# Optimization experiments

Measured on AMD Instinct MI355X. Metric: run time of the kernel, lower is better.

The kernel has to match this reference:

```python
import jax, jax.numpy as jnp
import numpy as np

NX = NY = 2048
DT = 0.01
DX = 1.0
DY = 1.0
RE = 1.0
NLEVEL = int(np.log2(NY)) + 1  # 12 levels


def pad_zero(x):
    # Dirichlet (zero) halo of width 1: matches boundary_condition_u/v/k/cw
    return jnp.pad(x, ((0, 0), (0, 0), (1, 1), (1, 1)))


def pad_edge(x):
    # Edge-replicate halo (incl. corners): matches boundary_condition_p
    return jnp.pad(x, ((0, 0), (0, 0), (1, 1), (1, 1)), mode='edge')


def conv2d(x, w, stride=1):
    return jax.lax.conv_general_dilated(
        x, w, (stride, stride), 'VALID',
        dimension_numbers=('NCHW', 'OIHW', 'NCHW'))


def upsample2(x):
    return jnp.repeat(jnp.repeat(x, 2, axis=2), 2, axis=3)


def pg_vector(u, v, pad_u, pad_v, k1, ADx_u, ADy_u, ADx_v, ADy_v, AD2_u, AD2_v, w_diff):
    # Petrov-Galerkin dissipation. pad_u/pad_v are the padded ORIGINAL velocities:
    # the torch code references the global values_uu/values_vv buffers here.
    k_u = 0.25 * DX * jnp.abs(0.5 * DX ** -3 * (jnp.abs(u) * DX + jnp.abs(v) * DY) * AD2_u) \
        / (0.001 + (jnp.abs(ADx_u) * DX ** -3 + jnp.abs(ADy_u) * DX ** -3) / 2.0)
    k_v = 0.25 * DY * jnp.abs(0.5 * DX ** -3 * (jnp.abs(u) * DX + jnp.abs(v) * DY) * AD2_v) \
        / (0.001 + (jnp.abs(ADx_v) * DX ** -3 + jnp.abs(ADy_v) * DX ** -3) / 2.0)
    k_u = jnp.minimum(k_u, k1)
    k_v = jnp.minimum(k_v, k1)
    k_uu = pad_zero(k_u)
    k_vv = pad_zero(k_v)
    k_x = 1.5 * (k_u * AD2_u + conv2d(pad_u * k_uu, w_diff) - u * conv2d(k_uu, w_diff))
    k_y = 1.5 * (k_v * AD2_v + conv2d(pad_v * k_vv, w_diff) - v * conv2d(k_vv, w_diff))
    return k_x, k_y


def f_cycle_mg(pad_u, pad_v, values_p, iteration, w_A, w_res, w_xadv, w_yadv):
    diag = w_A[0, 0, 1, 1]
    b = -(conv2d(pad_u, w_xadv) + conv2d(pad_v, w_yadv)) / DT
    w = jnp.zeros((1, 1, 2, 2), values_p.dtype)
    r = b
    for _ in range(iteration):
        w = jnp.zeros((1, 1, 2, 2), values_p.dtype)
        r = conv2d(pad_edge(values_p), w_A) - b
        r_s = [r]
        for _i in range(1, NLEVEL - 1):
            r = conv2d(r, w_res, stride=2)  # restriction down to 2x2
            r_s.append(r)
        for i in reversed(range(1, NLEVEL - 1)):
            w = w - conv2d(pad_zero(w), w_A) / diag + r_s[i] / diag  # Jacobi smooth
            w = upsample2(w)  # prolongation
        values_p = values_p - w
        values_p = values_p - conv2d(pad_edge(values_p), w_A) / diag + b / diag
    return values_p, w, r


def setup_inputs() -> dict:
    key = jax.random.key(0)
    ku, kv, kp = jax.random.split(key, 3)
    shp = (1, 1, NY, NX)
    f32 = jnp.float32
    values_u = jax.random.normal(ku, shp, f32) * 0.1
    values_v = jax.random.normal(kv, shp, f32) * 0.1
    values_p = jax.random.normal(kp, shp, f32) * 0.1
    Fx = jnp.zeros(shp, f32)
    Fy = jnp.zeros(shp, f32)
    k1 = jnp.ones(shp, f32) * (DX ** 2 / DT)
    # FD stencils (learned conv params in the torch module)
    w_xadv = jnp.array([[0., 0., 0.], [-0.5, 0., 0.5], [0., 0., 0.]], f32).reshape(1, 1, 3, 3) / DX
    w_yadv = jnp.array([[0., -0.5, 0.], [0., 0., 0.], [0., 0.5, 0.]], f32).reshape(1, 1, 3, 3) / DY
    lap = jnp.array([[0., 1., 0.], [1., -4., 1.], [0., 1., 0.]], f32).reshape(1, 1, 3, 3) / DX ** 2
    w_diff = lap
    w_A = lap  # diag = -4
    w_res = jnp.full((1, 1, 2, 2), 0.25, f32)
    return dict(values_u=values_u, values_v=values_v, values_p=values_p,
                Fx=Fx, Fy=Fy, k1=k1,
                w_xadv=w_xadv, w_yadv=w_yadv, w_diff=w_diff, w_A=w_A, w_res=w_res,
                iteration=5)


def reference(values_u, values_v, values_p, Fx, Fy, k1,
              w_xadv, w_yadv, w_diff, w_A, w_res, iteration):
    pad_u = pad_zero(values_u)
    pad_v = pad_zero(values_v)
    pad_p = pad_edge(values_p)
    Grapx_p = conv2d(pad_p, w_xadv) * DT
    Grapy_p = conv2d(pad_p, w_yadv) * DT
    ADx_u = conv2d(pad_u, w_xadv); ADy_u = conv2d(pad_u, w_yadv)
    ADx_v = conv2d(pad_v, w_xadv); ADy_v = conv2d(pad_v, w_yadv)
    AD2_u = conv2d(pad_u, w_diff); AD2_v = conv2d(pad_v, w_diff)
    k_x, k_y = pg_vector(values_u, values_v, pad_u, pad_v, k1,
                         ADx_u, ADy_u, ADx_v, ADy_v, AD2_u, AD2_v, w_diff)
    b_u = values_u + 0.5 * (RE * k_x * DT - values_u * ADx_u * DT - values_v * ADy_u * DT) - Grapx_p - Fx * DT * 0
    b_v = values_v + 0.5 * (RE * k_y * DT - values_u * ADx_v * DT - values_v * ADy_v * DT) - Grapy_p - Fy * DT * 0
    pad_bu = pad_zero(b_u)
    pad_bv = pad_zero(b_v)
    ADx_u = conv2d(pad_bu, w_xadv); ADy_u = conv2d(pad_bu, w_yadv)
    ADx_v = conv2d(pad_bv, w_xadv); ADy_v = conv2d(pad_bv, w_yadv)
    AD2_u = conv2d(pad_bu, w_diff); AD2_v = conv2d(pad_bv, w_diff)
    # torch code closes over the global padded ORIGINAL velocities here (pad_u, pad_v)
    k_x, k_y = pg_vector(b_u, b_v, pad_u, pad_v, k1,
                         ADx_u, ADy_u, ADx_v, ADy_v, AD2_u, AD2_v, w_diff)
    values_u = values_u + RE * k_x * DT - b_u * ADx_u * DT - b_v * ADy_u * DT - Grapx_p - Fx * DT
    values_v = values_v + RE * k_y * DT - b_u * ADx_v * DT - b_v * ADy_v * DT - Grapy_p - Fy * DT
    values_p, w, r = f_cycle_mg(pad_zero(values_u), pad_zero(values_v), values_p,
                                iteration, w_A, w_res, w_xadv, w_yadv)
    pad_p2 = pad_edge(values_p)
    values_u = values_u - conv2d(pad_p2, w_xadv) * DT
    values_v = values_v - conv2d(pad_p2, w_yadv) * DT
    return values_u, values_v, values_p, w, r
```

## Files before the change

kernel.cpp:

```cpp
#include <hip/hip_runtime.h>

#define NN 2048
#define NN2 (NN * NN)

__device__ __forceinline__ void load6z(const float* __restrict__ A, int i, int j0, float a[6]) {
    if ((unsigned)i >= (unsigned)NN) {
#pragma unroll
        for (int q = 0; q < 6; ++q) a[q] = 0.f;
        return;
    }
    const float* row = A + (size_t)i * NN;
    float4 c = *reinterpret_cast<const float4*>(row + j0);
    a[1] = c.x; a[2] = c.y; a[3] = c.z; a[4] = c.w;
    a[0] = (j0 > 0) ? row[j0 - 1] : 0.f;
    a[5] = (j0 + 4 < NN) ? row[j0 + 4] : 0.f;
}
__device__ __forceinline__ void load4z(const float* __restrict__ A, int i, int j0, float a[4]) {
    if ((unsigned)i >= (unsigned)NN) {
#pragma unroll
        for (int q = 0; q < 4; ++q) a[q] = 0.f;
        return;
    }
    float4 c = *reinterpret_cast<const float4*>(A + (size_t)i * NN + j0);
    a[0] = c.x; a[1] = c.y; a[2] = c.z; a[3] = c.w;
}
__device__ __forceinline__ void load6e(const float* __restrict__ A, int i, int j0, float a[6]) {
    i = i < 0 ? 0 : (i > NN - 1 ? NN - 1 : i);
    const float* row = A + (size_t)i * NN;
    float4 c = *reinterpret_cast<const float4*>(row + j0);
    a[1] = c.x; a[2] = c.y; a[3] = c.z; a[4] = c.w;
    a[0] = (j0 > 0) ? row[j0 - 1] : c.x;
    a[5] = (j0 + 4 < NN) ? row[j0 + 4] : c.w;
}
__device__ __forceinline__ void load4e(const float* __restrict__ A, int i, int j0, float a[4]) {
    i = i < 0 ? 0 : (i > NN - 1 ? NN - 1 : i);
    float4 c = *reinterpret_cast<const float4*>(A + (size_t)i * NN + j0);
    a[0] = c.x; a[1] = c.y; a[2] = c.z; a[3] = c.w;
}
__device__ __forceinline__ void store4(float* __restrict__ A, int i, int j0, const float a[4]) {
    *reinterpret_cast<float4*>(A + (size_t)i * NN + j0) = make_float4(a[0], a[1], a[2], a[3]);
}

__global__ __launch_bounds__(256) void k_pred_f(const float* __restrict__ u, const float* __restrict__ v,
                                                const float* __restrict__ k1, const float* __restrict__ p,
                                                float* __restrict__ bu, float* __restrict__ bv) {
    const float DT = 0.01f;
    __shared__ __align__(16) float su[36][72], sv[36][72];
    __shared__ float sku[34][68], skv[34][68];
    const int jb = blockIdx.x * 64;
    const int ib = blockIdx.y * 32;
    const int tid = threadIdx.y * 16 + threadIdx.x;

    for (int idx = tid; idx < 36 * 18; idx += 256) {
        int r = idx / 18, c4 = idx - r * 18;
        int gi = ib - 2 + r;
        int gj = jb - 4 + c4 * 4;
        float4 uu = make_float4(0.f, 0.f, 0.f, 0.f), vv = uu;
        if ((unsigned)gi < (unsigned)NN) {
            if (gj >= 0 && gj + 3 < NN) {
                uu = *reinterpret_cast<const float4*>(u + (size_t)gi * NN + gj);
                vv = *reinterpret_cast<const float4*>(v + (size_t)gi * NN + gj);
            } else {
                float tu[4], tv[4];
#pragma unroll
                for (int q = 0; q < 4; ++q) {
                    int g = gj + q;
                    bool in = (unsigned)g < (unsigned)NN;
                    tu[q] = in ? u[(size_t)gi * NN + g] : 0.f;
                    tv[q] = in ? v[(size_t)gi * NN + g] : 0.f;
                }
                uu = make_float4(tu[0], tu[1], tu[2], tu[3]);
                vv = make_float4(tv[0], tv[1], tv[2], tv[3]);
            }
        }
        *reinterpret_cast<float4*>(&su[r][c4 * 4]) = uu;
        *reinterpret_cast<float4*>(&sv[r][c4 * 4]) = vv;
    }
    __syncthreads();

    for (int idx = tid; idx < 34 * 66; idx += 256) {
        int r = idx / 66, c = idx - r * 66;
        int gi = ib - 1 + r, gj = jb - 1 + c;
        float kuo = 0.f, kvo = 0.f;
        if ((unsigned)gi < (unsigned)NN && (unsigned)gj < (unsigned)NN) {
            int lr = r + 1, lc = c + 3;
            float uc = su[lr][lc], ul = su[lr][lc - 1], ur = su[lr][lc + 1], ut = su[lr - 1][lc], ub = su[lr + 1][lc];
            float vc = sv[lr][lc], vl = sv[lr][lc - 1], vr = sv[lr][lc + 1], vt = sv[lr - 1][lc], vb = sv[lr + 1][lc];
            float ADxu = 0.5f * (ur - ul), ADyu = 0.5f * (ub - ut);
            float ADxv = 0.5f * (vr - vl), ADyv = 0.5f * (vb - vt);
            float Lu = ul + ur + ut + ub - 4.f * uc;
            float Lv = vl + vr + vt + vb - 4.f * vc;
            float s = fabsf(uc) + fabsf(vc);
            float kuv = 0.25f * fabsf(0.5f * s * Lu) / (0.001f + 0.5f * (fabsf(ADxu) + fabsf(ADyu)));
            float kvv = 0.25f * fabsf(0.5f * s * Lv) / (0.001f + 0.5f * (fabsf(ADxv) + fabsf(ADyv)));
            float k1c = k1[(size_t)gi * NN + gj];
            kuo = fminf(kuv, k1c);
            kvo = fminf(kvv, k1c);
        }
        sku[r][c] = kuo;
        skv[r][c] = kvo;
    }
    __syncthreads();

    const int i0 = ib + threadIdx.y * 2;
    const int j0 = jb + threadIdx.x * 4;
#pragma unroll
    for (int a = 0; a < 2; ++a) {
        int i = i0 + a;
        float p6[6], pu[4], pd[4], obu[4], obv[4];
        load6e(p, i, j0, p6); load4e(p, i - 1, j0, pu); load4e(p, i + 1, j0, pd);
        int lur = i - ib + 2, lkr = i - ib + 1;
#pragma unroll
        for (int c = 0; c < 4; ++c) {
            int luc = j0 + c - jb + 4, lkc = j0 + c - jb + 1;
            float uc = su[lur][luc], ul = su[lur][luc - 1], ur = su[lur][luc + 1], ut = su[lur - 1][luc], ub = su[lur + 1][luc];
            float vc = sv[lur][luc], vl = sv[lur][luc - 1], vr = sv[lur][luc + 1], vt = sv[lur - 1][luc], vb = sv[lur + 1][luc];
            float kuc = sku[lkr][lkc], kul = sku[lkr][lkc - 1], kur = sku[lkr][lkc + 1], kut = sku[lkr - 1][lkc], kub = sku[lkr + 1][lkc];
            float kvc = skv[lkr][lkc], kvl = skv[lkr][lkc - 1], kvr = skv[lkr][lkc + 1], kvt = skv[lkr - 1][lkc], kvb = skv[lkr + 1][lkc];
            float ADxu = 0.5f * (ur - ul), ADyu = 0.5f * (ub - ut);
            float ADxv = 0.5f * (vr - vl), ADyv = 0.5f * (vb - vt);
            float Lu = ul + ur + ut + ub - 4.f * uc;
            float Lv = vl + vr + vt + vb - 4.f * vc;
            float Lku = kul + kur + kut + kub - 4.f * kuc;
            float Lkv = kvl + kvr + kvt + kvb - 4.f * kvc;
            float Luku = ul * kul + ur * kur + ut * kut + ub * kub - 4.f * uc * kuc;
            float Lvkv = vl * kvl + vr * kvr + vt * kvt + vb * kvb - 4.f * vc * kvc;
            float kx = 1.5f * (kuc * Lu + Luku - uc * Lku);
            float ky = 1.5f * (kvc * Lv + Lvkv - vc * Lkv);
            float Grapx = 0.5f * (p6[c + 2] - p6[c]) * DT;
            float Grapy = 0.5f * (pd[c] - pu[c]) * DT;
            obu[c] = uc + 0.5f * (kx * DT - uc * ADxu * DT - vc * ADyu * DT) - Grapx;
            obv[c] = vc + 0.5f * (ky * DT - uc * ADxv * DT - vc * ADyv * DT) - Grapy;
        }
        store4(bu, i, j0, obu);
        store4(bv, i, j0, obv);
    }
}

__global__ __launch_bounds__(256) void k_corr_f(const float* __restrict__ u, const float* __restrict__ v,
                                                const float* __restrict__ k1, const float* __restrict__ p,
                                                const float* __restrict__ bu, const float* __restrict__ bv,
                                                const float* __restrict__ Fx, const float* __restrict__ Fy,
                                                float* __restrict__ un, float* __restrict__ vn) {
    const float DT = 0.01f;
    __shared__ __align__(16) float sbu[36][72], sbv[36][72];
    __shared__ float sku[34][68], skv[34][68];
    const int jb = blockIdx.x * 64;
    const int ib = blockIdx.y * 32;
    const int tid = threadIdx.y * 16 + threadIdx.x;

    for (int idx = tid; idx < 36 * 18; idx += 256) {
        int r = idx / 18, c4 = idx - r * 18;
        int gi = ib - 2 + r;
        int gj = jb - 4 + c4 * 4;
        float4 uu = make_float4(0.f, 0.f, 0.f, 0.f), vv = uu;
        if ((unsigned)gi < (unsigned)NN) {
            if (gj >= 0 && gj + 3 < NN) {
                uu = *reinterpret_cast<const float4*>(bu + (size_t)gi * NN + gj);
                vv = *reinterpret_cast<const float4*>(bv + (size_t)gi * NN + gj);
            } else {
                float tu[4], tv[4];
#pragma unroll
                for (int q = 0; q < 4; ++q) {
                    int g = gj + q;
                    bool in = (unsigned)g < (unsigned)NN;
                    tu[q] = in ? bu[(size_t)gi * NN + g] : 0.f;
                    tv[q] = in ? bv[(size_t)gi * NN + g] : 0.f;
                }
                uu = make_float4(tu[0], tu[1], tu[2], tu[3]);
                vv = make_float4(tv[0], tv[1], tv[2], tv[3]);
            }
        }
        *reinterpret_cast<float4*>(&sbu[r][c4 * 4]) = uu;
        *reinterpret_cast<float4*>(&sbv[r][c4 * 4]) = vv;
    }
    __syncthreads();

    for (int idx = tid; idx < 34 * 66; idx += 256) {
        int r = idx / 66, c = idx - r * 66;
        int gi = ib - 1 + r, gj = jb - 1 + c;
        float kuo = 0.f, kvo = 0.f;
        if ((unsigned)gi < (unsigned)NN && (unsigned)gj < (unsigned)NN) {
            int lr = r + 1, lc = c + 3;
            float uc = sbu[lr][lc], ul = sbu[lr][lc - 1], ur = sbu[lr][lc + 1], ut = sbu[lr - 1][lc], ub = sbu[lr + 1][lc];
            float vc = sbv[lr][lc], vl = sbv[lr][lc - 1], vr = sbv[lr][lc + 1], vt = sbv[lr - 1][lc], vb = sbv[lr + 1][lc];
            float ADxu = 0.5f * (ur - ul), ADyu = 0.5f * (ub - ut);
            float ADxv = 0.5f * (vr - vl), ADyv = 0.5f * (vb - vt);
            float Lu = ul + ur + ut + ub - 4.f * uc;
            float Lv = vl + vr + vt + vb - 4.f * vc;
            float s = fabsf(uc) + fabsf(vc);
            float kuv = 0.25f * fabsf(0.5f * s * Lu) / (0.001f + 0.5f * (fabsf(ADxu) + fabsf(ADyu)));
            float kvv = 0.25f * fabsf(0.5f * s * Lv) / (0.001f + 0.5f * (fabsf(ADxv) + fabsf(ADyv)));
            float k1c = k1[(size_t)gi * NN + gj];
            kuo = fminf(kuv, k1c);
            kvo = fminf(kvv, k1c);
        }
        sku[r][c] = kuo;
        skv[r][c] = kvo;
    }
    __syncthreads();

    const int i0 = ib + threadIdx.y * 2;
    const int j0 = jb + threadIdx.x * 4;
#pragma unroll
    for (int a = 0; a < 2; ++a) {
        int i = i0 + a;
        float p6[6], pu[4], pd[4];
        float u6[6], uu[4], ud[4], v6[6], vu[4], vd[4], fx[4], fy[4], oun[4], ovn[4];
        load6e(p, i, j0, p6); load4e(p, i - 1, j0, pu); load4e(p, i + 1, j0, pd);
        load6z(u, i, j0, u6); load4z(u, i - 1, j0, uu); load4z(u, i + 1, j0, ud);
        load6z(v, i, j0, v6); load4z(v, i - 1, j0, vu); load4z(v, i + 1, j0, vd);
        load4z(Fx, i, j0, fx); load4z(Fy, i, j0, fy);
        int lbr = i - ib + 2, lkr = i - ib + 1;
#pragma unroll
        for (int c = 0; c < 4; ++c) {
            int lbc = j0 + c - jb + 4, lkc = j0 + c - jb + 1;
            float buc = sbu[lbr][lbc], bul = sbu[lbr][lbc - 1], bur = sbu[lbr][lbc + 1], but = sbu[lbr - 1][lbc], bub = sbu[lbr + 1][lbc];
            float bvc = sbv[lbr][lbc], bvl = sbv[lbr][lbc - 1], bvr = sbv[lbr][lbc + 1], bvt = sbv[lbr - 1][lbc], bvb = sbv[lbr + 1][lbc];
            float kuc = sku[lkr][lkc], kul = sku[lkr][lkc - 1], kur = sku[lkr][lkc + 1], kut = sku[lkr - 1][lkc], kub = sku[lkr + 1][lkc];
            float kvc = skv[lkr][lkc], kvl = skv[lkr][lkc - 1], kvr = skv[lkr][lkc + 1], kvt = skv[lkr - 1][lkc], kvb = skv[lkr + 1][lkc];
            float uc = u6[c + 1], ul = u6[c], ur = u6[c + 2], ut = uu[c], ub = ud[c];
            float vc = v6[c + 1], vl = v6[c], vr = v6[c + 2], vt = vu[c], vb = vd[c];
            float ADxbu = 0.5f * (bur - bul), ADybu = 0.5f * (bub - but);
            float ADxbv = 0.5f * (bvr - bvl), ADybv = 0.5f * (bvb - bvt);
            float Lbu = bul + bur + but + bub - 4.f * buc;
            float Lbv = bvl + bvr + bvt + bvb - 4.f * bvc;
            float Lku = kul + kur + kut + kub - 4.f * kuc;
            float Lkv = kvl + kvr + kvt + kvb - 4.f * kvc;
            float Luku = ul * kul + ur * kur + ut * kut + ub * kub - 4.f * uc * kuc;
            float Lvkv = vl * kvl + vr * kvr + vt * kvt + vb * kvb - 4.f * vc * kvc;
            float kx = 1.5f * (kuc * Lbu + Luku - buc * Lku);
            float ky = 1.5f * (kvc * Lbv + Lvkv - bvc * Lkv);
            float Grapx = 0.5f * (p6[c + 2] - p6[c]) * DT;
            float Grapy = 0.5f * (pd[c] - pu[c]) * DT;
            oun[c] = uc + kx * DT - buc * ADxbu * DT - bvc * ADybu * DT - Grapx - fx[c] * DT;
            ovn[c] = vc + ky * DT - buc * ADxbv * DT - bvc * ADybv * DT - Grapy - fy[c] * DT;
        }
        store4(un, i, j0, oun);
        store4(vn, i, j0, ovn);
    }
}

__global__ __launch_bounds__(256) void k_rhs_v(const float* __restrict__ un, const float* __restrict__ vn,
                                               float* __restrict__ b) {
    const float INVDT = 100.0f;
    int jt = blockIdx.x * blockDim.x + threadIdx.x;
    int i  = blockIdx.y * blockDim.y + threadIdx.y;
    int j0 = jt * 4;
    float u6[6], vu[4], vd[4], ob[4];
    load6z(un, i, j0, u6);
    load4z(vn, i - 1, j0, vu); load4z(vn, i + 1, j0, vd);
#pragma unroll
    for (int c = 0; c < 4; ++c) {
        float adx = 0.5f * (u6[c + 2] - u6[c]);
        float ady = 0.5f * (vd[c] - vu[c]);
        ob[c] = -(adx + ady) * INVDT;
    }
    store4(b, i, j0, ob);
}

__global__ __launch_bounds__(256) void k_resrestrict(const float* __restrict__ p, const float* __restrict__ b,
                                                     float* __restrict__ r1024, float* __restrict__ r512,
                                                     float* __restrict__ r256, float* __restrict__ r128) {
    __shared__ float s512[4][64];
    __shared__ float s256[2][32];
    int tx = threadIdx.x, ty = threadIdx.y;
    int jt = blockIdx.x * 64 + tx;
    int it = blockIdx.y * 4 + ty;
    int j0 = jt * 4, i0 = it * 4;
    float p6[6][6];
#pragma unroll
    for (int r = 0; r < 6; ++r) load6e(p, i0 - 1 + r, j0, p6[r]);
    float res[4][4];
#pragma unroll
    for (int r = 0; r < 4; ++r) {
        float bb[4];
        load4z(b, i0 + r, j0, bb);
#pragma unroll
        for (int c = 0; c < 4; ++c) {
            float pc = p6[r + 1][c + 1];
            float nb = p6[r][c + 1] + p6[r + 2][c + 1] + p6[r + 1][c] + p6[r + 1][c + 2];
            res[r][c] = nb - 4.f * pc - bb[c];
        }
    }
    float q00 = 0.25f * (res[0][0] + res[0][1] + res[1][0] + res[1][1]);
    float q01 = 0.25f * (res[0][2] + res[0][3] + res[1][2] + res[1][3]);
    float q10 = 0.25f * (res[2][0] + res[2][1] + res[3][0] + res[3][1]);
    float q11 = 0.25f * (res[2][2] + res[2][3] + res[3][2] + res[3][3]);
    int ci = it * 2, cj = jt * 2;
    *reinterpret_cast<float2*>(r1024 + (size_t)ci * 1024 + cj)       = make_float2(q00, q01);
    *reinterpret_cast<float2*>(r1024 + (size_t)(ci + 1) * 1024 + cj) = make_float2(q10, q11);
    float s = 0.25f * (q00 + q01 + q10 + q11);
    r512[(size_t)it * 512 + jt] = s;
    s512[ty][tx] = s;
    __syncthreads();
    int tid = ty * 64 + tx;
    if (tid < 64) {
        int a = tid >> 5, c = tid & 31;
        float m = 0.25f * (s512[2 * a][2 * c] + s512[2 * a][2 * c + 1] + s512[2 * a + 1][2 * c] + s512[2 * a + 1][2 * c + 1]);
        r256[(size_t)(blockIdx.y * 2 + a) * 256 + blockIdx.x * 32 + c] = m;
        s256[a][c] = m;
    }
    __syncthreads();
    if (tid < 16) {
        float m = 0.25f * (s256[0][2 * tid] + s256[0][2 * tid + 1] + s256[1][2 * tid] + s256[1][2 * tid + 1]);
        r128[(size_t)blockIdx.y * 128 + blockIdx.x * 16 + tid] = m;
    }
}

__global__ __launch_bounds__(1024) void k_small(const float* __restrict__ r128,
                                                float* __restrict__ w128_out,
                                                float* __restrict__ r2_out) {
    __shared__ float sr64[64 * 64];
    __shared__ float sr32[32 * 32];
    __shared__ float sr16[16 * 16];
    __shared__ float sr8[8 * 8];
    __shared__ float sr4[16];
    __shared__ float sr2[4];
    __shared__ float wa[64 * 64];
    __shared__ float wb[64 * 64];
    int t = threadIdx.x;

    for (int idx = t; idx < 64 * 64; idx += 1024) {
        int i = idx >> 6, j = idx & 63;
        const float* s0 = r128 + (2 * i) * 128 + 2 * j;
        sr64[idx] = 0.25f * (s0[0] + s0[1] + s0[128] + s0[129]);
    }
    __syncthreads();
    if (t < 32 * 32) {
        int i = t >> 5, j = t & 31;
        const float* s0 = sr64 + (2 * i) * 64 + 2 * j;
        sr32[t] = 0.25f * (s0[0] + s0[1] + s0[64] + s0[65]);
    }
    __syncthreads();
    if (t < 16 * 16) {
        int i = t >> 4, j = t & 15;
        const float* s0 = sr32 + (2 * i) * 32 + 2 * j;
        sr16[t] = 0.25f * (s0[0] + s0[1] + s0[32] + s0[33]);
    }
    __syncthreads();
    if (t < 64) {
        int i = t >> 3, j = t & 7;
        const float* s0 = sr16 + (2 * i) * 16 + 2 * j;
        sr8[t] = 0.25f * (s0[0] + s0[1] + s0[16] + s0[17]);
    }
    __syncthreads();
    if (t < 16) {
        int i = t >> 2, j = t & 3;
        const float* s0 = sr8 + (2 * i) * 8 + 2 * j;
        sr4[t] = 0.25f * (s0[0] + s0[1] + s0[8] + s0[9]);
    }
    __syncthreads();
    if (t < 4) {
        int i = t >> 1, j = t & 1;
        const float* s0 = sr4 + (2 * i) * 4 + 2 * j;
        sr2[t] = 0.25f * (s0[0] + s0[1] + s0[4] + s0[5]);
        r2_out[t] = sr2[t];
        float ws = -0.25f * sr2[t];
        wa[(2 * i) * 4 + 2 * j] = ws;
        wa[(2 * i) * 4 + 2 * j + 1] = ws;
        wa[(2 * i + 1) * 4 + 2 * j] = ws;
        wa[(2 * i + 1) * 4 + 2 * j + 1] = ws;
    }
    __syncthreads();

    auto step = [&](const float* win, const float* rl, float* wout, int s) {
        for (int idx = t; idx < s * s; idx += 1024) {
            int i = idx / s, j = idx - i * s;
            float up = i > 0 ? win[(i - 1) * s + j] : 0.f;
            float dn = i < s - 1 ? win[(i + 1) * s + j] : 0.f;
            float lf = j > 0 ? win[i * s + j - 1] : 0.f;
            float rt = j < s - 1 ? win[i * s + j + 1] : 0.f;
            float ws = 0.25f * (up + dn + lf + rt - rl[idx]);
            int o = 2 * s;
            wout[(2 * i) * o + 2 * j] = ws;
            wout[(2 * i) * o + 2 * j + 1] = ws;
            wout[(2 * i + 1) * o + 2 * j] = ws;
            wout[(2 * i + 1) * o + 2 * j + 1] = ws;
        }
    };
    step(wa, sr4, wb, 4);
    __syncthreads();
    step(wb, sr8, wa, 8);
    __syncthreads();
    step(wa, sr16, wb, 16);
    __syncthreads();
    step(wb, sr32, wa, 32);
    __syncthreads();
    step(wa, sr64, w128_out, 64);
}

__global__ __launch_bounds__(256) void k_prolong(const float* __restrict__ win, const float* __restrict__ rl,
                                                 float* __restrict__ wout, int n) {
    int j = blockIdx.x * blockDim.x + threadIdx.x;
    int i = blockIdx.y * blockDim.y + threadIdx.y;
    float up = i > 0 ? win[(i - 1) * n + j] : 0.f;
    float dn = i < n - 1 ? win[(i + 1) * n + j] : 0.f;
    float lf = j > 0 ? win[i * n + j - 1] : 0.f;
    float rt = j < n - 1 ? win[i * n + j + 1] : 0.f;
    float ws = 0.25f * (up + dn + lf + rt - rl[i * n + j]);
    int o = 2 * n;
    float2 vv = make_float2(ws, ws);
    *reinterpret_cast<float2*>(wout + (2 * i) * o + 2 * j) = vv;
    *reinterpret_cast<float2*>(wout + (2 * i + 1) * o + 2 * j) = vv;
}

template <bool LAST>
__global__ __launch_bounds__(256) void k_pupd2(const float* __restrict__ p, const float* __restrict__ b,
                                               const float* __restrict__ w512, const float* __restrict__ r512,
                                               const float* __restrict__ r1024,
                                               float* __restrict__ pdst, float* __restrict__ wout) {
    __shared__ float sW[6][72];
    __shared__ float sS[4][68];
    __shared__ float ws[4][130];
    const int jb = blockIdx.x * 256;
    const int ib = blockIdx.y * 4;
    const int cr_base = ib / 2 - 1;
    const int cc_base = jb / 2 - 1;
    const int sr_base = (ib / 2 - 2) >> 1;
    const int sc_base = (jb / 2 - 2) >> 1;
    const int wr_base = sr_base - 1, wc_base = sc_base - 1;
    const int tid = threadIdx.y * 64 + threadIdx.x;

    for (int idx = tid; idx < 6 * 68; idx += 256) {
        int r = idx / 68, c = idx - r * 68;
        int gi = wr_base + r, gj = wc_base + c;
        sW[r][c] = ((unsigned)gi < 512u && (unsigned)gj < 512u) ? w512[(size_t)gi * 512 + gj] : 0.f;
    }
    __syncthreads();
    for (int idx = tid; idx < 4 * 66; idx += 256) {
        int r = idx / 66, c = idx - r * 66;
        int gi = sr_base + r, gj = sc_base + c;
        float val = 0.f;
        if ((unsigned)gi < 512u && (unsigned)gj < 512u) {
            int lr = r + 1, lc = c + 1;
            val = 0.25f * (sW[lr - 1][lc] + sW[lr + 1][lc] + sW[lr][lc - 1] + sW[lr][lc + 1]
                           - r512[(size_t)gi * 512 + gj]);
        }
        sS[r][c] = val;
    }
    __syncthreads();
    for (int idx = tid; idx < 4 * 130; idx += 256) {
        int r = idx / 130, c = idx - r * 130;
        int ci = cr_base + r, cj = cc_base + c;
        float val = 0.f;
        if ((unsigned)ci < 1024u && (unsigned)cj < 1024u) {
            float nsum = 0.f;
            {
                int R = ci - 1, C = cj;
                if ((unsigned)R < 1024u) nsum += sS[(R >> 1) - sr_base][(C >> 1) - sc_base];
            }
            {
                int R = ci + 1, C = cj;
                if ((unsigned)R < 1024u) nsum += sS[(R >> 1) - sr_base][(C >> 1) - sc_base];
            }
            {
                int R = ci, C = cj - 1;
                if ((unsigned)C < 1024u) nsum += sS[(R >> 1) - sr_base][(C >> 1) - sc_base];
            }
            {
                int R = ci, C = cj + 1;
                if ((unsigned)C < 1024u) nsum += sS[(R >> 1) - sr_base][(C >> 1) - sc_base];
            }
            val = 0.25f * (nsum - r1024[(size_t)ci * 1024 + cj]);
        }
        ws[r][c] = val;
    }
    __syncthreads();

    const int i  = ib + threadIdx.y;
    const int j0 = jb + threadIdx.x * 4;
    float p6[6], pu[4], pd[4], bb[4], op[4];
    load6e(p, i, j0, p6);
    load4e(p, i - 1, j0, pu);
    load4e(p, i + 1, j0, pd);
    load4z(b, i, j0, bb);

    const int iu = (i - 1) < 0 ? 0 : (i - 1);
    const int id = (i + 1) > NN - 1 ? NN - 1 : (i + 1);
    const int lrC = (i >> 1) - cr_base;
    const int lrU = (iu >> 1) - cr_base;
    const int lrD = (id >> 1) - cr_base;

#pragma unroll
    for (int c = 0; c < 4; ++c) {
        int f = j0 + c;
        int fl = (f - 1) < 0 ? 0 : (f - 1);
        int fr = (f + 1) > NN - 1 ? NN - 1 : (f + 1);
        float pml = p6[c]     - ws[lrC][(fl >> 1) - cc_base];
        float pmr = p6[c + 2] - ws[lrC][(fr >> 1) - cc_base];
        float pmt = pu[c]     - ws[lrU][(f >> 1) - cc_base];
        float pmb = pd[c]     - ws[lrD][(f >> 1) - cc_base];
        op[c] = 0.25f * (pml + pmr + pmt + pmb - bb[c]);
    }
    store4(pdst, i, j0, op);
    if (LAST) {
        float ow[4];
#pragma unroll
        for (int c = 0; c < 4; ++c) ow[c] = ws[lrC][((j0 + c) >> 1) - cc_base];
        store4(wout, i, j0, ow);
    }
}

__global__ __launch_bounds__(256) void k_fcorr_v(const float* __restrict__ p,
                                                 float* __restrict__ un, float* __restrict__ vn) {
    const float DT = 0.01f;
    int jt = blockIdx.x * blockDim.x + threadIdx.x;
    int i  = blockIdx.y * blockDim.y + threadIdx.y;
    int j0 = jt * 4;
    float p6[6], pu[4], pd[4];
    load6e(p, i, j0, p6);
    load4e(p, i - 1, j0, pu);
    load4e(p, i + 1, j0, pd);
    float4 uc = *reinterpret_cast<float4*>(un + (size_t)i * NN + j0);
    float4 vc = *reinterpret_cast<float4*>(vn + (size_t)i * NN + j0);
    float ou[4] = {uc.x, uc.y, uc.z, uc.w};
    float ov[4] = {vc.x, vc.y, vc.z, vc.w};
#pragma unroll
    for (int c = 0; c < 4; ++c) {
        ou[c] -= 0.5f * (p6[c + 2] - p6[c]) * DT;
        ov[c] -= 0.5f * (pd[c] - pu[c]) * DT;
    }
    store4(un, i, j0, ou);
    store4(vn, i, j0, ov);
}

extern "C" void kernel_launch(void* const* d_in, const int* in_sizes, int n_in,
                              void* d_out, int out_size, void* d_ws, size_t ws_size,
                              hipStream_t stream) {
    const float* u  = (const float*)d_in[0];
    const float* v  = (const float*)d_in[1];
    const float* p  = (const float*)d_in[2];
    const float* Fx = (const float*)d_in[3];
    const float* Fy = (const float*)d_in[4];
    const float* k1 = (const float*)d_in[5];

    float* out = (float*)d_out;
    float* out_u = out;
    float* out_v = out + (size_t)NN2;
    float* out_p = out + 2 * (size_t)NN2;
    float* out_w = out + 3 * (size_t)NN2;
    float* out_r = out + 4 * (size_t)NN2;

    float* ws = (float*)d_ws;
    float* b  = ws;
    float* pA = ws + (size_t)NN2;
    float* pB = ws + 2 * (size_t)NN2;
    float* r1024 = ws + 3 * (size_t)NN2;
    float* r512  = r1024 + 1024 * 1024;
    float* r256  = r512 + 512 * 512;
    float* r128  = r256 + 256 * 256;
    float* w128  = r128 + 128 * 128;
    float* w256  = w128 + 128 * 128;
    float* w512  = w256 + 256 * 256;

    float* bu = out_w;
    float* bv = out_p;

    dim3 blk(64, 4);
    dim3 g4(8, 512);
    dim3 blkT(16, 16);
    dim3 gT(32, 64);

    k_pred_f<<<gT, blkT, 0, stream>>>(u, v, k1, p, bu, bv);
    k_corr_f<<<gT, blkT, 0, stream>>>(u, v, k1, p, bu, bv, Fx, Fy, out_u, out_v);
    k_rhs_v<<<g4, blk, 0, stream>>>(out_u, out_v, b);

    const float* pcur = p;
    for (int it = 0; it < 5; ++it) {
        k_resrestrict<<<dim3(8, 128), blk, 0, stream>>>(pcur, b, r1024, r512, r256, r128);
        k_small<<<1, 1024, 0, stream>>>(r128, w128, out_r);
        k_prolong<<<dim3(2, 32), blk, 0, stream>>>(w128, r128, w256, 128);
        k_prolong<<<dim3(4, 64), blk, 0, stream>>>(w256, r256, w512, 256);
        if (it < 4) {
            float* pdst = (it & 1) ? pB : pA;
            k_pupd2<false><<<dim3(8, 512), blk, 0, stream>>>(pcur, b, w512, r512, r1024, pdst, nullptr);
            pcur = pdst;
        } else {
            k_pupd2<true><<<dim3(8, 512), blk, 0, stream>>>(pcur, b, w512, r512, r1024, out_p, out_w);
        }
    }

    k_fcorr_v<<<g4, blk, 0, stream>>>(out_p, out_u, out_v);
}
```

Before: 400.8 us.

## Fuse multigrid prolongation, pressure update and next-residual restriction into one kernel

Merges the RHS build with the first residual/restriction pass. It also folds the two prolongation kernels, the pressure update, the next iteration's residual restriction and the final velocity correction into a single tiled kernel per V-cycle. Each block recomputes the coarse-level corrections it needs from w128 in shared memory, using 16-row tiles with halos. Residual pyramids are ping-ponged between two buffer sets. This removes several launches and full-grid round trips of p and the residuals, at the cost of more redundant halo recomputation and heavy shared-memory use that may lower occupancy.

```diff
diff --git a/kernel.cpp b/kernel.cpp
--- a/kernel.cpp
+++ b/kernel.cpp
@@ -241,48 +241,39 @@
     }
 }
 
-__global__ __launch_bounds__(256) void k_rhs_v(const float* __restrict__ un, const float* __restrict__ vn,
-                                               float* __restrict__ b) {
-    const float INVDT = 100.0f;
-    int jt = blockIdx.x * blockDim.x + threadIdx.x;
-    int i  = blockIdx.y * blockDim.y + threadIdx.y;
-    int j0 = jt * 4;
-    float u6[6], vu[4], vd[4], ob[4];
-    load6z(un, i, j0, u6);
-    load4z(vn, i - 1, j0, vu); load4z(vn, i + 1, j0, vd);
-#pragma unroll
-    for (int c = 0; c < 4; ++c) {
-        float adx = 0.5f * (u6[c + 2] - u6[c]);
-        float ady = 0.5f * (vd[c] - vu[c]);
-        ob[c] = -(adx + ady) * INVDT;
-    }
-    store4(b, i, j0, ob);
-}
-
-__global__ __launch_bounds__(256) void k_resrestrict(const float* __restrict__ p, const float* __restrict__ b,
-                                                     float* __restrict__ r1024, float* __restrict__ r512,
-                                                     float* __restrict__ r256, float* __restrict__ r128) {
-    __shared__ float s512[4][64];
-    __shared__ float s256[2][32];
+__global__ __launch_bounds__(256) void k_rhs_res(const float* __restrict__ un, const float* __restrict__ vn,
+                                                 const float* __restrict__ p, float* __restrict__ b,
+                                                 float* __restrict__ r1024, float* __restrict__ r512,
+                                                 float* __restrict__ r256, float* __restrict__ r128) {
+    __shared__ float s512r[4][64];
+    __shared__ float s256r[2][32];
     int tx = threadIdx.x, ty = threadIdx.y;
     int jt = blockIdx.x * 64 + tx;
     int it = blockIdx.y * 4 + ty;
     int j0 = jt * 4, i0 = it * 4;
+    float bb[4][4];
+#pragma unroll
+    for (int r = 0; r < 4; ++r) {
+        float u6[6], vu[4], vd[4];
+        load6z(un, i0 + r, j0, u6);
+        load4z(vn, i0 + r - 1, j0, vu);
+        load4z(vn, i0 + r + 1, j0, vd);
+#pragma unroll
+        for (int c = 0; c < 4; ++c)
+            bb[r][c] = -100.f * (0.5f * (u6[c + 2] - u6[c]) + 0.5f * (vd[c] - vu[c]));
+        store4(b, i0 + r, j0, bb[r]);
+    }
     float p6[6][6];
 #pragma unroll
     for (int r = 0; r < 6; ++r) load6e(p, i0 - 1 + r, j0, p6[r]);
     float res[4][4];
 #pragma unroll
-    for (int r = 0; r < 4; ++r) {
-        float bb[4];
-        load4z(b, i0 + r, j0, bb);
+    for (int r = 0; r < 4; ++r)
 #pragma unroll
         for (int c = 0; c < 4; ++c) {
             float pc = p6[r + 1][c + 1];
-            float nb = p6[r][c + 1] + p6[r + 2][c + 1] + p6[r + 1][c] + p6[r + 1][c + 2];
-            res[r][c] = nb - 4.f * pc - bb[c];
-        }
-    }
+            res[r][c] = p6[r][c + 1] + p6[r + 2][c + 1] + p6[r + 1][c] + p6[r + 1][c + 2] - 4.f * pc - bb[r][c];
+        }
     float q00 = 0.25f * (res[0][0] + res[0][1] + res[1][0] + res[1][1]);
     float q01 = 0.25f * (res[0][2] + res[0][3] + res[1][2] + res[1][3]);
     float q10 = 0.25f * (res[2][0] + res[2][1] + res[3][0] + res[3][1]);
@@ -292,18 +283,18 @@
     *reinterpret_cast<float2*>(r1024 + (size_t)(ci + 1) * 1024 + cj) = make_float2(q10, q11);
     float s = 0.25f * (q00 + q01 + q10 + q11);
     r512[(size_t)it * 512 + jt] = s;
-    s512[ty][tx] = s;
+    s512r[ty][tx] = s;
     __syncthreads();
     int tid = ty * 64 + tx;
     if (tid < 64) {
         int a = tid >> 5, c = tid & 31;
-        float m = 0.25f * (s512[2 * a][2 * c] + s512[2 * a][2 * c + 1] + s512[2 * a + 1][2 * c] + s512[2 * a + 1][2 * c + 1]);
+        float m = 0.25f * (s512r[2 * a][2 * c] + s512r[2 * a][2 * c + 1] + s512r[2 * a + 1][2 * c] + s512r[2 * a + 1][2 * c + 1]);
         r256[(size_t)(blockIdx.y * 2 + a) * 256 + blockIdx.x * 32 + c] = m;
-        s256[a][c] = m;
+        s256r[a][c] = m;
     }
     __syncthreads();
     if (tid < 16) {
-        float m = 0.25f * (s256[0][2 * tid] + s256[0][2 * tid + 1] + s256[1][2 * tid] + s256[1][2 * tid + 1]);
+        float m = 0.25f * (s256r[0][2 * tid] + s256r[0][2 * tid + 1] + s256r[1][2 * tid] + s256r[1][2 * tid + 1]);
         r128[(size_t)blockIdx.y * 128 + blockIdx.x * 16 + tid] = m;
     }
 }
@@ -390,139 +381,231 @@
     step(wa, sr64, w128_out, 64);
 }
 
-__global__ __launch_bounds__(256) void k_prolong(const float* __restrict__ win, const float* __restrict__ rl,
-                                                 float* __restrict__ wout, int n) {
-    int j = blockIdx.x * blockDim.x + threadIdx.x;
-    int i = blockIdx.y * blockDim.y + threadIdx.y;
-    float up = i > 0 ? win[(i - 1) * n + j] : 0.f;
-    float dn = i < n - 1 ? win[(i + 1) * n + j] : 0.f;
-    float lf = j > 0 ? win[i * n + j - 1] : 0.f;
-    float rt = j < n - 1 ? win[i * n + j + 1] : 0.f;
-    float ws = 0.25f * (up + dn + lf + rt - rl[i * n + j]);
-    int o = 2 * n;
-    float2 vv = make_float2(ws, ws);
-    *reinterpret_cast<float2*>(wout + (2 * i) * o + 2 * j) = vv;
-    *reinterpret_cast<float2*>(wout + (2 * i + 1) * o + 2 * j) = vv;
-}
-
 template <bool LAST>
-__global__ __launch_bounds__(256) void k_pupd2(const float* __restrict__ p, const float* __restrict__ b,
-                                               const float* __restrict__ w512, const float* __restrict__ r512,
-                                               const float* __restrict__ r1024,
-                                               float* __restrict__ pdst, float* __restrict__ wout) {
-    __shared__ float sW[6][72];
-    __shared__ float sS[4][68];
-    __shared__ float ws[4][130];
+__global__ __launch_bounds__(256) void k_mg_step(
+    const float* __restrict__ p, const float* __restrict__ b,
+    const float* __restrict__ w128,
+    const float* __restrict__ r128, const float* __restrict__ r256,
+    const float* __restrict__ r512, const float* __restrict__ r1024,
+    float* __restrict__ pdst,
+    float* __restrict__ o1024, float* __restrict__ o512,
+    float* __restrict__ o256, float* __restrict__ o128,
+    float* __restrict__ wout, float* __restrict__ un, float* __restrict__ vn)
+{
+    __shared__ float sw128[5][20];
+    __shared__ float s128[3][18];
+    __shared__ float s256[4][34];
+    __shared__ float s512[6][66];
+    __shared__ float s1024[10][132];
+    __shared__ __align__(16) float pmid[20][264];
+    __shared__ float pnew[18][258];
+    __shared__ float red512[4][64];
+    __shared__ float red256[2][32];
+
     const int jb = blockIdx.x * 256;
-    const int ib = blockIdx.y * 4;
-    const int cr_base = ib / 2 - 1;
-    const int cc_base = jb / 2 - 1;
-    const int sr_base = (ib / 2 - 2) >> 1;
-    const int sc_base = (jb / 2 - 2) >> 1;
-    const int wr_base = sr_base - 1, wc_base = sc_base - 1;
+    const int ib = blockIdx.y * 16;
     const int tid = threadIdx.y * 64 + threadIdx.x;
-
-    for (int idx = tid; idx < 6 * 68; idx += 256) {
-        int r = idx / 68, c = idx - r * 68;
-        int gi = wr_base + r, gj = wc_base + c;
-        sW[r][c] = ((unsigned)gi < 512u && (unsigned)gj < 512u) ? w512[(size_t)gi * 512 + gj] : 0.f;
-    }
-    __syncthreads();
-    for (int idx = tid; idx < 4 * 66; idx += 256) {
-        int r = idx / 66, c = idx - r * 66;
-        int gi = sr_base + r, gj = sc_base + c;
-        float val = 0.f;
-        if ((unsigned)gi < 512u && (unsigned)gj < 512u) {
-            int lr = r + 1, lc = c + 1;
-            val = 0.25f * (sW[lr - 1][lc] + sW[lr + 1][lc] + sW[lr][lc - 1] + sW[lr][lc + 1]
-                           - r512[(size_t)gi * 512 + gj]);
-        }
-        sS[r][c] = val;
-    }
-    __syncthreads();
-    for (int idx = tid; idx < 4 * 130; idx += 256) {
-        int r = idx / 130, c = idx - r * 130;
-        int ci = cr_base + r, cj = cc_base + c;
-        float val = 0.f;
-        if ((unsigned)ci < 1024u && (unsigned)cj < 1024u) {
-            float nsum = 0.f;
-            {
-                int R = ci - 1, C = cj;
-                if ((unsigned)R < 1024u) nsum += sS[(R >> 1) - sr_base][(C >> 1) - sc_base];
+    const int r1 = ib / 2 - 1,  c1 = jb / 2 - 1;
+    const int r2 = ib / 4 - 1,  c2 = jb / 4 - 1;
+    const int r3 = ib / 8 - 1,  c3 = jb / 8 - 1;
+    const int r4 = ib / 16 - 1, c4 = jb / 16 - 1;
+    const int r5 = ib / 16 - 2, c5 = jb / 16 - 2;
+
+    if (tid < 100) {
+        int r = tid / 20, c = tid - (tid / 20) * 20;
+        int x = r5 + r, y = c5 + c;
+        sw128[r][c] = ((unsigned)x < 128u && (unsigned)y < 128u) ? w128[x * 128 + y] : 0.f;
+    }
+    __syncthreads();
+    if (tid < 54) {
+        int r = tid / 18, c = tid - (tid / 18) * 18;
+        int x = r4 + r, y = c4 + c;
+        float v = 0.f;
+        if ((unsigned)x < 128u && (unsigned)y < 128u) {
+            float s = 0.f;
+            if (x > 0)   s += sw128[r][c + 1];
+            if (x < 127) s += sw128[r + 2][c + 1];
+            if (y > 0)   s += sw128[r + 1][c];
+            if (y < 127) s += sw128[r + 1][c + 2];
+            v = 0.25f * (s - r128[x * 128 + y]);
+        }
+        s128[r][c] = v;
+    }
+    __syncthreads();
+    if (tid < 136) {
+        int r = tid / 34, c = tid - (tid / 34) * 34;
+        int x = r3 + r, y = c3 + c;
+        float v = 0.f;
+        if ((unsigned)x < 256u && (unsigned)y < 256u) {
+            float s = 0.f;
+            if (x > 0)   s += s128[((x - 1) >> 1) - r4][(y >> 1) - c4];
+            if (x < 255) s += s128[((x + 1) >> 1) - r4][(y >> 1) - c4];
+            if (y > 0)   s += s128[(x >> 1) - r4][((y - 1) >> 1) - c4];
+            if (y < 255) s += s128[(x >> 1) - r4][((y + 1) >> 1) - c4];
+            v = 0.25f * (s - r256[x * 256 + y]);
+        }
+        s256[r][c] = v;
+    }
+    __syncthreads();
+    for (int idx = tid; idx < 6 * 66; idx += 256) {
+        int r = idx / 66, c = idx - (idx / 66) * 66;
+        int x = r2 + r, y = c2 + c;
+        float v = 0.f;
+        if ((unsigned)x < 512u && (unsigned)y < 512u) {
+            float s = 0.f;
+            if (x > 0)   s += s256[((x - 1) >> 1) - r3][(y >> 1) - c3];
+            if (x < 511) s += s256[((x + 1) >> 1) - r3][(y >> 1) - c3];
+            if (y > 0)   s += s256[(x >> 1) - r3][((y - 1) >> 1) - c3];
+            if (y < 511) s += s256[(x >> 1) - r3][((y + 1) >> 1) - c3];
+            v = 0.25f * (s - r512[x * 512 + y]);
+        }
+        s512[r][c] = v;
+    }
+    __syncthreads();
+    for (int idx = tid; idx < 10 * 130; idx += 256) {
+        int r = idx / 130, c = idx - (idx / 130) * 130;
+        int x = r1 + r, y = c1 + c;
+        float v = 0.f;
+        if ((unsigned)x < 1024u && (unsigned)y < 1024u) {
+            float s = 0.f;
+            if (x > 0)    s += s512[((x - 1) >> 1) - r2][(y >> 1) - c2];
+            if (x < 1023) s += s512[((x + 1) >> 1) - r2][(y >> 1) - c2];
+            if (y > 0)    s += s512[(x >> 1) - r2][((y - 1) >> 1) - c2];
+            if (y < 1023) s += s512[(x >> 1) - r2][((y + 1) >> 1) - c2];
+            v = 0.25f * (s - r1024[x * 1024 + y]);
+        }
+        s1024[r][c] = v;
+    }
+    __syncthreads();
+    for (int idx = tid; idx < 20 * 66; idx += 256) {
+        int r = idx / 66, q = idx - (idx / 66) * 66;
+        int gi = ib - 2 + r;
+        int gj0 = jb - 4 + q * 4;
+        float vals[4] = {0.f, 0.f, 0.f, 0.f};
+        if ((unsigned)gi < (unsigned)NN) {
+            if (gj0 >= 0 && gj0 + 3 < NN) {
+                float4 pv = *reinterpret_cast<const float4*>(p + (size_t)gi * NN + gj0);
+                vals[0] = pv.x; vals[1] = pv.y; vals[2] = pv.z; vals[3] = pv.w;
+            } else {
+#pragma unroll
+                for (int q4 = 0; q4 < 4; ++q4) {
+                    int gj = gj0 + q4;
+                    vals[q4] = ((unsigned)gj < (unsigned)NN) ? p[(size_t)gi * NN + gj] : 0.f;
+                }
             }
-            {
-                int R = ci + 1, C = cj;
-                if ((unsigned)R < 1024u) nsum += sS[(R >> 1) - sr_base][(C >> 1) - sc_base];
+        }
+#pragma unroll
+        for (int q4 = 0; q4 < 4; ++q4) {
+            int gj = gj0 + q4;
+            float m = 0.f;
+            if ((unsigned)gi < (unsigned)NN && (unsigned)gj < (unsigned)NN &&
+                gj >= jb - 2 && gj <= jb + 257) {
+                m = vals[q4] - s1024[(gi >> 1) - r1][(gj >> 1) - c1];
             }
-            {
-                int R = ci, C = cj - 1;
-                if ((unsigned)C < 1024u) nsum += sS[(R >> 1) - sr_base][(C >> 1) - sc_base];
+            pmid[r][q * 4 + q4] = m;
+        }
+    }
+    __syncthreads();
+    for (int idx = tid; idx < 18 * 258; idx += 256) {
+        int r = idx / 258, c = idx - (idx / 258) * 258;
+        int gi = ib - 1 + r, gj = jb - 1 + c;
+        float v = 0.f;
+        if ((unsigned)gi < (unsigned)NN && (unsigned)gj < (unsigned)NN) {
+            int iu = gi > 0 ? gi - 1 : 0;
+            int idn = gi < NN - 1 ? gi + 1 : NN - 1;
+            int jl = gj > 0 ? gj - 1 : 0;
+            int jr = gj < NN - 1 ? gj + 1 : NN - 1;
+            float s = pmid[iu - (ib - 2)][gj - (jb - 4)] + pmid[idn - (ib - 2)][gj - (jb - 4)]
+                    + pmid[gi - (ib - 2)][jl - (jb - 4)] + pmid[gi - (ib - 2)][jr - (jb - 4)];
+            v = 0.25f * (s - b[(size_t)gi * NN + gj]);
+        }
+        pnew[r][c] = v;
+    }
+    __syncthreads();
+
+    const int i0 = ib + threadIdx.y * 4;
+    const int j0 = jb + threadIdx.x * 4;
+#pragma unroll
+    for (int rr = 0; rr < 4; ++rr) {
+        int i = i0 + rr;
+        int lr = i - (ib - 1);
+        int lc = j0 - (jb - 1);
+        *reinterpret_cast<float4*>(pdst + (size_t)i * NN + j0) =
+            make_float4(pnew[lr][lc], pnew[lr][lc + 1], pnew[lr][lc + 2], pnew[lr][lc + 3]);
+    }
+
+    if (LAST) {
+        const float DT = 0.01f;
+#pragma unroll
+        for (int rr = 0; rr < 4; ++rr) {
+            int i = i0 + rr;
+            int lr = i - (ib - 1);
+            int s1r = (i >> 1) - r1;
+            float ow[4];
+#pragma unroll
+            for (int c = 0; c < 4; ++c) ow[c] = s1024[s1r][((j0 + c) >> 1) - c1];
+            store4(wout, i, j0, ow);
+            float4 uu = *reinterpret_cast<float4*>(un + (size_t)i * NN + j0);
+            float4 vv = *reinterpret_cast<float4*>(vn + (size_t)i * NN + j0);
+            float ou[4] = {uu.x, uu.y, uu.z, uu.w};
+            float ov[4] = {vv.x, vv.y, vv.z, vv.w};
+            int iu = (i > 0 ? i - 1 : 0) - (ib - 1);
+            int idn = (i < NN - 1 ? i + 1 : NN - 1) - (ib - 1);
+#pragma unroll
+            for (int c = 0; c < 4; ++c) {
+                int j = j0 + c;
+                int jl = (j > 0 ? j - 1 : 0) - (jb - 1);
+                int jr = (j < NN - 1 ? j + 1 : NN - 1) - (jb - 1);
+                int lc = j - (jb - 1);
+                ou[c] -= 0.5f * (pnew[lr][jr] - pnew[lr][jl]) * DT;
+                ov[c] -= 0.5f * (pnew[idn][lc] - pnew[iu][lc]) * DT;
             }
-            {
-                int R = ci, C = cj + 1;
-                if ((unsigned)C < 1024u) nsum += sS[(R >> 1) - sr_base][(C >> 1) - sc_base];
+            store4(un, i, j0, ou);
+            store4(vn, i, j0, ov);
+        }
+    } else {
+        float res[4][4];
+#pragma unroll
+        for (int rr = 0; rr < 4; ++rr) {
+#pragma unroll
+            for (int cc = 0; cc < 4; ++cc) {
+                int i = i0 + rr, j = j0 + cc;
+                int lr = i - (ib - 1), lc = j - (jb - 1);
+                int iu = (i > 0 ? i - 1 : 0) - (ib - 1);
+                int idn = (i < NN - 1 ? i + 1 : NN - 1) - (ib - 1);
+                int jl = (j > 0 ? j - 1 : 0) - (jb - 1);
+                int jr = (j < NN - 1 ? j + 1 : NN - 1) - (jb - 1);
+                res[rr][cc] = pnew[iu][lc] + pnew[idn][lc] + pnew[lr][jl] + pnew[lr][jr]
+                            - 4.f * pnew[lr][lc] - b[(size_t)i * NN + j];
             }
-            val = 0.25f * (nsum - r1024[(size_t)ci * 1024 + cj]);
-        }
-        ws[r][c] = val;
-    }
-    __syncthreads();
-
-    const int i  = ib + threadIdx.y;
-    const int j0 = jb + threadIdx.x * 4;
-    float p6[6], pu[4], pd[4], bb[4], op[4];
-    load6e(p, i, j0, p6);
-    load4e(p, i - 1, j0, pu);
-    load4e(p, i + 1, j0, pd);
-    load4z(b, i, j0, bb);
-
-    const int iu = (i - 1) < 0 ? 0 : (i - 1);
-    const int id = (i + 1) > NN - 1 ? NN - 1 : (i + 1);
-    const int lrC = (i >> 1) - cr_base;
-    const int lrU = (iu >> 1) - cr_base;
-    const int lrD = (id >> 1) - cr_base;
-
-#pragma unroll
-    for (int c = 0; c < 4; ++c) {
-        int f = j0 + c;
-        int fl = (f - 1) < 0 ? 0 : (f - 1);
-        int fr = (f + 1) > NN - 1 ? NN - 1 : (f + 1);
-        float pml = p6[c]     - ws[lrC][(fl >> 1) - cc_base];
-        float pmr = p6[c + 2] - ws[lrC][(fr >> 1) - cc_base];
-        float pmt = pu[c]     - ws[lrU][(f >> 1) - cc_base];
-        float pmb = pd[c]     - ws[lrD][(f >> 1) - cc_base];
-        op[c] = 0.25f * (pml + pmr + pmt + pmb - bb[c]);
-    }
-    store4(pdst, i, j0, op);
-    if (LAST) {
-        float ow[4];
-#pragma unroll
-        for (int c = 0; c < 4; ++c) ow[c] = ws[lrC][((j0 + c) >> 1) - cc_base];
-        store4(wout, i, j0, ow);
-    }
-}
-
-__global__ __launch_bounds__(256) void k_fcorr_v(const float* __restrict__ p,
-                                                 float* __restrict__ un, float* __restrict__ vn) {
-    const float DT = 0.01f;
-    int jt = blockIdx.x * blockDim.x + threadIdx.x;
-    int i  = blockIdx.y * blockDim.y + threadIdx.y;
-    int j0 = jt * 4;
-    float p6[6], pu[4], pd[4];
-    load6e(p, i, j0, p6);
-    load4e(p, i - 1, j0, pu);
-    load4e(p, i + 1, j0, pd);
-    float4 uc = *reinterpret_cast<float4*>(un + (size_t)i * NN + j0);
-    float4 vc = *reinterpret_cast<float4*>(vn + (size_t)i * NN + j0);
-    float ou[4] = {uc.x, uc.y, uc.z, uc.w};
-    float ov[4] = {vc.x, vc.y, vc.z, vc.w};
-#pragma unroll
-    for (int c = 0; c < 4; ++c) {
-        ou[c] -= 0.5f * (p6[c + 2] - p6[c]) * DT;
-        ov[c] -= 0.5f * (pd[c] - pu[c]) * DT;
-    }
-    store4(un, i, j0, ou);
-    store4(vn, i, j0, ov);
+        }
+        int it = blockIdx.y * 4 + threadIdx.y;
+        int jt = blockIdx.x * 64 + threadIdx.x;
+        float q00 = 0.25f * (res[0][0] + res[0][1] + res[1][0] + res[1][1]);
+        float q01 = 0.25f * (res[0][2] + res[0][3] + res[1][2] + res[1][3]);
+        float q10 = 0.25f * (res[2][0] + res[2][1] + res[3][0] + res[3][1]);
+        float q11 = 0.25f * (res[2][2] + res[2][3] + res[3][2] + res[3][3]);
+        int ci = it * 2, cj = jt * 2;
+        *reinterpret_cast<float2*>(o1024 + (size_t)ci * 1024 + cj)       = make_float2(q00, q01);
+        *reinterpret_cast<float2*>(o1024 + (size_t)(ci + 1) * 1024 + cj) = make_float2(q10, q11);
+        float s = 0.25f * (q00 + q01 + q10 + q11);
+        o512[(size_t)it * 512 + jt] = s;
+        red512[threadIdx.y][threadIdx.x] = s;
+        __syncthreads();
+        if (tid < 64) {
+            int a = tid >> 5, c = tid & 31;
+            float m = 0.25f * (red512[2 * a][2 * c] + red512[2 * a][2 * c + 1] +
+                               red512[2 * a + 1][2 * c] + red512[2 * a + 1][2 * c + 1]);
+            o256[(size_t)(blockIdx.y * 2 + a) * 256 + blockIdx.x * 32 + c] = m;
+            red256[a][c] = m;
+        }
+        __syncthreads();
+        if (tid < 16) {
+            float m = 0.25f * (red256[0][2 * tid] + red256[0][2 * tid + 1] +
+                               red256[1][2 * tid] + red256[1][2 * tid + 1]);
+            o128[(size_t)blockIdx.y * 128 + blockIdx.x * 16 + tid] = m;
+        }
+    }
 }
 
 extern "C" void kernel_launch(void* const* d_in, const int* in_sizes, int n_in,
@@ -546,40 +629,52 @@
     float* b  = ws;
     float* pA = ws + (size_t)NN2;
     float* pB = ws + 2 * (size_t)NN2;
-    float* r1024 = ws + 3 * (size_t)NN2;
-    float* r512  = r1024 + 1024 * 1024;
-    float* r256  = r512 + 512 * 512;
-    float* r128  = r256 + 256 * 256;
-    float* w128  = r128 + 128 * 128;
-    float* w256  = w128 + 128 * 128;
-    float* w512  = w256 + 256 * 256;
+    float* base = ws + 3 * (size_t)NN2;
+    float* rA1024 = base;
+    float* rA512  = rA1024 + 1024 * 1024;
+    float* rA256  = rA512 + 512 * 512;
+    float* rA128  = rA256 + 256 * 256;
+    float* rB1024 = rA128 + 128 * 128;
+    float* rB512  = rB1024 + 1024 * 1024;
+    float* rB256  = rB512 + 512 * 512;
+    float* rB128  = rB256 + 256 * 256;
+    float* w128   = rB128 + 128 * 128;
 
     float* bu = out_w;
     float* bv = out_p;
 
     dim3 blk(64, 4);
-    dim3 g4(8, 512);
     dim3 blkT(16, 16);
     dim3 gT(32, 64);
+    dim3 gM(8, 128);
 
     k_pred_f<<<gT, blkT, 0, stream>>>(u, v, k1, p, bu, bv);
     k_corr_f<<<gT, blkT, 0, stream>>>(u, v, k1, p, bu, bv, Fx, Fy, out_u, out_v);
-    k_rhs_v<<<g4, blk, 0, stream>>>(out_u, out_v, b);
+    k_rhs_res<<<gM, blk, 0, stream>>>(out_u, out_v, p, b, rA1024, rA512, rA256, rA128);
 
     const float* pcur = p;
     for (int it = 0; it < 5; ++it) {
-        k_resrestrict<<<dim3(8, 128), blk, 0, stream>>>(pcur, b, r1024, r512, r256, r128);
-        k_small<<<1, 1024, 0, stream>>>(r128, w128, out_r);
-        k_prolong<<<dim3(2, 32), blk, 0, stream>>>(w128, r128, w256, 128);
-        k_prolong<<<dim3(4, 64), blk, 0, stream>>>(w256, r256, w512, 256);
+        const bool useA = (it % 2 == 0);
+        const float* R1024 = useA ? rA1024 : rB1024;
+        const float* R512  = useA ? rA512  : rB512;
+        const float* R256  = useA ? rA256  : rB256;
+        const float* R128  = useA ? rA128  : rB128;
+        float* O1024 = useA ? rB1024 : rA1024;
+        float* O512  = useA ? rB512  : rA512;
+        float* O256  = useA ? rB256  : rA256;
+        float* O128  = useA ? rB128  : rA128;
+
+        k_small<<<1, 1024, 0, stream>>>(R128, w128, out_r);
         if (it < 4) {
             float* pdst = (it & 1) ? pB : pA;
-            k_pupd2<false><<<dim3(8, 512), blk, 0, stream>>>(pcur, b, w512, r512, r1024, pdst, nullptr);
+            k_mg_step<false><<<gM, blk, 0, stream>>>(pcur, b, w128, R128, R256, R512, R1024,
+                                                     pdst, O1024, O512, O256, O128,
+                                                     nullptr, nullptr, nullptr);
             pcur = pdst;
         } else {
-            k_pupd2<true><<<dim3(8, 512), blk, 0, stream>>>(pcur, b, w512, r512, r1024, out_p, out_w);
-        }
-    }
-
-    k_fcorr_v<<<g4, blk, 0, stream>>>(out_p, out_u, out_v);
-}
+            k_mg_step<true><<<gM, blk, 0, stream>>>(pcur, b, w128, R128, R256, R512, R1024,
+                                                    out_p, nullptr, nullptr, nullptr, nullptr,
+                                                    out_w, out_u, out_v);
+        }
+    }
+}
```

New measurement: 459.1 us. 1.15x slower.
